# Kernel optimization log

Hardware: AMD Instinct MI355X
Metric: run time of the kernel (lower is better)

## Reference

```python
import jax, jax.numpy as jnp
import numpy as np

B, N, D, H, WIN = 8, 4096, 768, 8, 8
HD = D // H
FG = N // 2 + 1
FL = WIN // 2 + 1


def _gelu(x):
    return jax.nn.gelu(x, approximate=False)


def _cgelu(z):
    # magnitude-based complex GELU: z * gelu(|z|) / (|z| + 1e-6)
    mag = jnp.abs(z)
    return z * (_gelu(mag) / (mag + 1e-6))


def setup_inputs():
    key = jax.random.key(0)
    ks = jax.random.split(key, 8)

    def w(k, shape):
        return jax.random.normal(k, shape, dtype=jnp.float32) * 0.02

    return {
        "x": jax.random.normal(ks[0], (B, N, D), dtype=jnp.float32),
        "ln_w": jnp.ones((D,), jnp.float32),
        "ln_b": jnp.zeros((D,), jnp.float32),
        "bf_g": jnp.ones((H, FG, 1), jnp.float32),
        "bb_g": jnp.full((H, FG, 1), -0.1, jnp.float32),
        "bf_l": jnp.ones((H, FL, 1), jnp.float32),
        "bb_l": jnp.full((H, FL, 1), -0.1, jnp.float32),
        "w1g": w(ks[1], (D, D)),
        "b1g": jnp.zeros((D,), jnp.float32),
        "w2g": w(ks[2], (D, H * FG * 2)),
        "b2g": jnp.zeros((H * FG * 2,), jnp.float32),
        "w1l": w(ks[3], (D, D)),
        "b1l": jnp.zeros((D,), jnp.float32),
        "w2l": w(ks[4], (D, H * FL * 2)),
        "b2l": jnp.zeros((H * FL * 2,), jnp.float32),
        "wf1": w(ks[5], (D, D // 2)),
        "bf1": jnp.zeros((D // 2,), jnp.float32),
        "wf2": w(ks[6], (D // 2, H)),
        "bf2": jnp.zeros((H,), jnp.float32),
    }


def reference(x, ln_w, ln_b, bf_g, bb_g, bf_l, bb_l, w1g, b1g, w2g, b2g,
              w1l, b1l, w2l, b2l, wf1, bf1, wf2, bf2):
    # pre-norm (LayerNorm, eps=1e-5)
    mu = jnp.mean(x, axis=-1, keepdims=True)
    var = jnp.mean((x - mu) ** 2, axis=-1, keepdims=True)
    xn = (x - mu) / jnp.sqrt(var + 1e-5) * ln_w + ln_b
    xh = xn.reshape(B, N, H, HD).transpose(0, 2, 1, 3)  # (B,H,N,HD)
    ctx = xn.mean(axis=1)  # (B,D)

    # ---- global branch: Hann-windowed rFFT over full sequence ----
    ag = (_gelu(ctx @ w1g + b1g) @ w2g + b2g).reshape(B, H, FG, 2)
    hann_g = jnp.hanning(N).astype(x.dtype)[None, None, :, None]
    Ff = jnp.fft.rfft(xh * hann_g, axis=2, norm="ortho")  # (B,H,FG,HD) complex
    eff_f = bf_g[None] * (1.0 + ag[..., 0:1])
    eff_b = bb_g[None] + ag[..., 1:2]
    x_global = jnp.fft.irfft(_cgelu(Ff * eff_f + eff_b), n=N, axis=2, norm="ortho")

    al = (_gelu(ctx @ w1l + b1l) @ w2l + b2l).reshape(B, H, FL, 2)
    nw = N // WIN
    hann_l = jnp.hanning(WIN).astype(x.dtype)[None, None, None, :, None]
    xw = xh.reshape(B, H, nw, WIN, HD) * hann_l
    Fl_fft = jnp.fft.rfft(xw, axis=3, norm="ortho")  # (B,H,nw,FL,HD)
    eff_fl = bf_l[None, :, None] * (1.0 + al[:, :, None, :, 0:1])
    eff_bl = bb_l[None, :, None] + al[:, :, None, :, 1:2]
    x_local = jnp.fft.irfft(_cgelu(Fl_fft * eff_fl + eff_bl), n=WIN, axis=3,
                            norm="ortho").reshape(B, H, N, HD)

    # ---- fusion gate ----
    alpha = jax.nn.sigmoid(_gelu(ctx @ wf1 + bf1) @ wf2 + bf2).reshape(B, H, 1, 1)
    fused = alpha * x_global + (1.0 - alpha) * x_local
    return x + fused.transpose(0, 2, 1, 3).reshape(B, N, D)
```

## Files before the change

### kernel.cpp

```cpp
#include <hip/hip_runtime.h>
#include <math.h>

#define B_ 8
#define N_ 4096
#define D_ 768
#define H_ 8
#define HD_ 96
#define FG_ 2049
#define TWO_PI 6.283185307179586476925f
#define SWZ(i) ((i) ^ (((i) >> 4) & 15))

__device__ __forceinline__ float erf_fast(float x) {
    float ax = fabsf(x);
    float t = __builtin_amdgcn_rcpf(fmaf(0.3275911f, ax, 1.0f));
    float p = fmaf(fmaf(fmaf(fmaf(1.061405429f, t, -1.453152027f), t, 1.421413741f),
                        t, -0.284496736f), t, 0.254829592f) * t;
    float r = 1.0f - p * __expf(-ax * ax);
    return copysignf(r, x);
}

__device__ __forceinline__ float gelu_f(float x) {
    return 0.5f * x * (1.0f + erf_fast(x * 0.7071067811865475f));
}

__device__ __forceinline__ int rev4_12(int x) {
    int r = (int)(__brev((unsigned)x) >> 20);
    return ((r & 0x555) << 1) | ((r >> 1) & 0x555);
}

__global__ void k_init(const float* __restrict__ b2g, const float* __restrict__ b2l,
                       const float* __restrict__ b1g, const float* __restrict__ b1l,
                       float2* __restrict__ twg, float* __restrict__ hanng,
                       float* __restrict__ ctx, float* __restrict__ ag,
                       float* __restrict__ al, float* __restrict__ h1g,
                       float* __restrict__ h1l) {
    int i = blockIdx.x * 256 + threadIdx.x;
    if (i < 2048) {
        float s, c;
        sincosf(-TWO_PI * (float)i / 4096.0f, &s, &c);
        twg[i] = make_float2(c, s);
    }
    if (i < 4096) hanng[i] = 0.5f - 0.5f * cosf(TWO_PI * (float)i / 4095.0f);
    if (i < B_ * D_) ctx[i] = 0.f;
    if (i < 768) {
        float vg = b1g[i], vl = b1l[i];
        for (int b = 0; b < B_; ++b) {
            h1g[b * 768 + i] = vg;
            h1l[b * 768 + i] = vl;
        }
    }
    const int CG = H_ * FG_ * 2;
    if (i < CG) {
        float v = b2g[i];
        for (int b = 0; b < B_; ++b) ag[(size_t)b * CG + i] = v;
    } else if (i < CG + 80) {
        int cc = i - CG;
        float v = b2l[cc];
        for (int b = 0; b < B_; ++b) al[b * 80 + cc] = v;
    }
}

__global__ __launch_bounds__(256) void k_stats(const float* __restrict__ x,
                                               float* __restrict__ mu,
                                               float* __restrict__ rstd) {
    int row = blockIdx.x * 4 + (threadIdx.x >> 6);
    int lane = threadIdx.x & 63;
    const float4* xr = (const float4*)(x + (size_t)row * D_);
    float4 a = xr[lane], b = xr[lane + 64], c = xr[lane + 128];
    float s = a.x + a.y + a.z + a.w + b.x + b.y + b.z + b.w + c.x + c.y + c.z + c.w;
    #pragma unroll
    for (int o = 32; o > 0; o >>= 1) s += __shfl_xor(s, o);
    float m = s * (1.0f / 768.0f);
    float v = 0.f, d;
    d = a.x - m; v += d * d; d = a.y - m; v += d * d;
    d = a.z - m; v += d * d; d = a.w - m; v += d * d;
    d = b.x - m; v += d * d; d = b.y - m; v += d * d;
    d = b.z - m; v += d * d; d = b.w - m; v += d * d;
    d = c.x - m; v += d * d; d = c.y - m; v += d * d;
    d = c.z - m; v += d * d; d = c.w - m; v += d * d;
    #pragma unroll
    for (int o = 32; o > 0; o >>= 1) v += __shfl_xor(v, o);
    if (lane == 0) {
        mu[row] = m;
        rstd[row] = rsqrtf(v * (1.0f / 768.0f) + 1e-5f);
    }
}

__global__ __launch_bounds__(256) void k_lnT(const float* __restrict__ x,
                                             const float* __restrict__ mu,
                                             const float* __restrict__ rstd,
                                             const float* __restrict__ lw,
                                             const float* __restrict__ lb,
                                             float* __restrict__ xt,
                                             float* __restrict__ ctx) {
    __shared__ float tile[64][65];
    __shared__ float csum[4][64];
    int d0 = blockIdx.x * 64, n0 = blockIdx.y * 64, b = blockIdx.z;
    int c = threadIdx.x & 63, r4 = threadIdx.x >> 6;
    float w = lw[d0 + c], bias = lb[d0 + c];
    float partial = 0.f;
    #pragma unroll
    for (int q = 0; q < 16; ++q) {
        int r = r4 * 16 + q;
        int row = b * N_ + n0 + r;
        float v = (x[(size_t)row * D_ + d0 + c] - mu[row]) * rstd[row] * w + bias;
        tile[r][c] = v;
        partial += v;
    }
    csum[r4][c] = partial;
    __syncthreads();
    if (r4 == 0)
        atomicAdd(ctx + b * D_ + d0 + c,
                  (csum[0][c] + csum[1][c] + csum[2][c] + csum[3][c]) * (1.0f / 4096.0f));
    #pragma unroll
    for (int q = 0; q < 16; ++q) {
        int r = r4 * 16 + q;
        xt[((size_t)b * D_ + d0 + r) * N_ + n0 + c] = tile[c][r];
    }
}

__global__ void k_mlp1(const float* __restrict__ ctx,
                       const float* __restrict__ w1g, const float* __restrict__ w1l,
                       const float* __restrict__ wf1, const float* __restrict__ bf1,
                       float* __restrict__ h1g, float* __restrict__ h1l,
                       float* __restrict__ hf) {
    int t = threadIdx.x, xb = blockIdx.x, y = blockIdx.y;
    float acc[B_];
    #pragma unroll
    for (int b = 0; b < B_; ++b) acc[b] = 0.f;
    if (y < 8) {
        int c = xb * 256 + t;
        if (c >= 1536) return;
        const float* w = (c < 768) ? w1g : w1l;
        float* out = (c < 768) ? h1g : h1l;
        int cc = (c < 768) ? c : c - 768;
        int d0 = y * 96;
        for (int d = 0; d < 96; ++d) {
            float wv = w[(size_t)(d0 + d) * 768 + cc];
            #pragma unroll
            for (int b = 0; b < B_; ++b) acc[b] += ctx[b * 768 + d0 + d] * wv;
        }
        for (int b = 0; b < B_; ++b) atomicAdd(out + b * 768 + cc, acc[b]);
    } else {
        if (xb < 6) return;
        int cc = (xb - 6) * 256 + t;
        if (cc >= 384) return;
        for (int d = 0; d < 768; ++d) {
            float wv = wf1[(size_t)d * 384 + cc];
            #pragma unroll
            for (int b = 0; b < B_; ++b) acc[b] += ctx[b * 768 + d] * wv;
        }
        float bv = bf1[cc];
        for (int b = 0; b < B_; ++b) hf[b * 384 + cc] = gelu_f(acc[b] + bv);
    }
}

__global__ void k_mlp2(const float* __restrict__ h1g, const float* __restrict__ h1l,
                       const float* __restrict__ hf,
                       const float* __restrict__ w2g, const float* __restrict__ w2l,
                       const float* __restrict__ wf2, const float* __restrict__ bf2,
                       float* __restrict__ ag, float* __restrict__ al, float* __restrict__ gate) {
    int kc = blockIdx.y;
    int d0 = kc * 96;
    __shared__ float lg[B_ * 96];
    __shared__ float ll[B_ * 96];
    for (int i = threadIdx.x; i < B_ * 96; i += 256) {
        int bb = i / 96, dd = i % 96;
        lg[i] = gelu_f(h1g[bb * 768 + d0 + dd]);
        ll[i] = gelu_f(h1l[bb * 768 + d0 + dd]);
    }
    __syncthreads();
    int c = blockIdx.x * 256 + threadIdx.x;
    const int CG = H_ * FG_ * 2;
    float acc[B_];
    #pragma unroll
    for (int b = 0; b < B_; ++b) acc[b] = 0.f;
    if (c < CG) {
        for (int d = 0; d < 96; ++d) {
            float wv = w2g[(size_t)(d0 + d) * CG + c];
            #pragma unroll
            for (int b = 0; b < B_; ++b) acc[b] += lg[b * 96 + d] * wv;
        }
        for (int b = 0; b < B_; ++b) atomicAdd(ag + (size_t)b * CG + c, acc[b]);
    } else if (c < CG + 80) {
        int cc = c - CG;
        for (int d = 0; d < 96; ++d) {
            float wv = w2l[(d0 + d) * 80 + cc];
            #pragma unroll
            for (int b = 0; b < B_; ++b) acc[b] += ll[b * 96 + d] * wv;
        }
        for (int b = 0; b < B_; ++b) atomicAdd(al + b * 80 + cc, acc[b]);
    } else if (c < CG + 88 && kc == 0) {
        int cc = c - CG - 80;
        for (int d = 0; d < 384; ++d) {
            float wv = wf2[d * 8 + cc];
            #pragma unroll
            for (int b = 0; b < B_; ++b) acc[b] += hf[b * 384 + d] * wv;
        }
        for (int b = 0; b < B_; ++b)
            gate[b * 8 + cc] = 1.0f / (1.0f + expf(-(acc[b] + bf2[cc])));
    }
}

template<int LQ>
__device__ __forceinline__ void dit_stage_f(float2* z, const float2* __restrict__ twg, int t) {
    const int Q = 1 << LQ;
    #pragma unroll
    for (int u = 0; u < 4; ++u) {
        int j = t + (u << 8);
        int pos = j & (Q - 1);
        int i0 = ((j >> LQ) << (LQ + 2)) + pos;
        int p0 = SWZ(i0), p1 = SWZ(i0 + Q), p2 = SWZ(i0 + 2 * Q), p3 = SWZ(i0 + 3 * Q);
        float2 a = z[p0], b = z[p1], c = z[p2], d = z[p3];
        float2 w1 = twg[pos << (10 - LQ)];
        float2 w2 = make_float2(w1.x * w1.x - w1.y * w1.y, 2.f * w1.x * w1.y);
        float2 w3 = make_float2(w1.x * w2.x - w1.y * w2.y, w1.x * w2.y + w1.y * w2.x);
        float2 bh = make_float2(b.x * w1.x - b.y * w1.y, b.x * w1.y + b.y * w1.x);
        float2 ch = make_float2(c.x * w2.x - c.y * w2.y, c.x * w2.y + c.y * w2.x);
        float2 dh = make_float2(d.x * w3.x - d.y * w3.y, d.x * w3.y + d.y * w3.x);
        float t0x = a.x + ch.x,  t0y = a.y + ch.y;
        float t1x = a.x - ch.x,  t1y = a.y - ch.y;
        float t2x = bh.x + dh.x, t2y = bh.y + dh.y;
        float t3x = bh.x - dh.x, t3y = bh.y - dh.y;
        z[p0] = make_float2(t0x + t2x, t0y + t2y);
        z[p1] = make_float2(t1x + t3y, t1y - t3x);
        z[p2] = make_float2(t0x - t2x, t0y - t2y);
        z[p3] = make_float2(t1x - t3y, t1y + t3x);
    }
}

template<int LQ>
__device__ __forceinline__ void dif_stage_i(float2* z, const float2* __restrict__ twg, int t) {
    const int Q = 1 << LQ;
    #pragma unroll
    for (int u = 0; u < 4; ++u) {
        int j = t + (u << 8);
        int pos = j & (Q - 1);
        int i0 = ((j >> LQ) << (LQ + 2)) + pos;
        int p0 = SWZ(i0), p1 = SWZ(i0 + Q), p2 = SWZ(i0 + 2 * Q), p3 = SWZ(i0 + 3 * Q);
        float2 a = z[p0], b = z[p1], c = z[p2], d = z[p3];
        float t0x = a.x + c.x,  t0y = a.y + c.y;
        float t1x = a.x - c.x,  t1y = a.y - c.y;
        float t2x = b.x + d.x,  t2y = b.y + d.y;
        float t3x = b.x - d.x,  t3y = b.y - d.y;
        float2 w1 = twg[pos << (10 - LQ)];
        w1.y = -w1.y;
        float2 w2 = make_float2(w1.x * w1.x - w1.y * w1.y, 2.f * w1.x * w1.y);
        float2 w3 = make_float2(w1.x * w2.x - w1.y * w2.y, w1.x * w2.y + w1.y * w2.x);
        z[p0] = make_float2(t0x + t2x, t0y + t2y);
        float y1x = t1x - t3y, y1y = t1y + t3x;
        z[p1] = make_float2(y1x * w1.x - y1y * w1.y, y1x * w1.y + y1y * w1.x);
        float y2x = t0x - t2x, y2y = t0y - t2y;
        z[p2] = make_float2(y2x * w2.x - y2y * w2.y, y2x * w2.y + y2y * w2.x);
        float y3x = t1x + t3y, y3y = t1y - t3x;
        z[p3] = make_float2(y3x * w3.x - y3y * w3.y, y3x * w3.y + y3y * w3.x);
    }
}

#define W16C_INIT {1.f, 0.9238795325f, 0.7071067812f, 0.3826834324f, 0.f, \
                   -0.3826834324f, -0.7071067812f, -0.9238795325f, -1.f, -0.9238795325f}
#define W16S_INIT {0.f, -0.3826834324f, -0.7071067812f, -0.9238795325f, -1.f, \
                   -0.9238795325f, -0.7071067812f, -0.3826834324f, 0.f, 0.3826834324f}

__device__ __forceinline__ void fwd16_dit(float2* v) {
    #pragma unroll
    for (int g = 0; g < 4; ++g) {
        float2 a = v[4*g], b = v[4*g+1], c = v[4*g+2], d = v[4*g+3];
        float t0x = a.x + c.x, t0y = a.y + c.y, t1x = a.x - c.x, t1y = a.y - c.y;
        float t2x = b.x + d.x, t2y = b.y + d.y, t3x = b.x - d.x, t3y = b.y - d.y;
        v[4*g]   = make_float2(t0x + t2x, t0y + t2y);
        v[4*g+1] = make_float2(t1x + t3y, t1y - t3x);
        v[4*g+2] = make_float2(t0x - t2x, t0y - t2y);
        v[4*g+3] = make_float2(t1x - t3y, t1y + t3x);
    }
    const float WC[10] = W16C_INIT;
    const float WS[10] = W16S_INIT;
    #pragma unroll
    for (int m = 0; m < 4; ++m) {
        float2 a = v[m];
        float2 b0 = v[m+4], c0 = v[m+8], d0 = v[m+12];
        float2 b = make_float2(b0.x*WC[m]   - b0.y*WS[m],   b0.x*WS[m]   + b0.y*WC[m]);
        float2 c = make_float2(c0.x*WC[2*m] - c0.y*WS[2*m], c0.x*WS[2*m] + c0.y*WC[2*m]);
        float2 d = make_float2(d0.x*WC[3*m] - d0.y*WS[3*m], d0.x*WS[3*m] + d0.y*WC[3*m]);
        float t0x = a.x + c.x, t0y = a.y + c.y, t1x = a.x - c.x, t1y = a.y - c.y;
        float t2x = b.x + d.x, t2y = b.y + d.y, t3x = b.x - d.x, t3y = b.y - d.y;
        v[m]    = make_float2(t0x + t2x, t0y + t2y);
        v[m+4]  = make_float2(t1x + t3y, t1y - t3x);
        v[m+8]  = make_float2(t0x - t2x, t0y - t2y);
        v[m+12] = make_float2(t1x - t3y, t1y + t3x);
    }
}

__device__ __forceinline__ void inv16_dif(float2* v) {
    const float WC[10] = W16C_INIT;
    const float WS[10] = W16S_INIT;
    #pragma unroll
    for (int m = 0; m < 4; ++m) {
        float2 a = v[m], b = v[m+4], c = v[m+8], d = v[m+12];
        float t0x = a.x + c.x, t0y = a.y + c.y, t1x = a.x - c.x, t1y = a.y - c.y;
        float t2x = b.x + d.x, t2y = b.y + d.y, t3x = b.x - d.x, t3y = b.y - d.y;
        float y1x = t1x - t3y, y1y = t1y + t3x;
        float y2x = t0x - t2x, y2y = t0y - t2y;
        float y3x = t1x + t3y, y3y = t1y - t3x;
        v[m]    = make_float2(t0x + t2x, t0y + t2y);
        v[m+4]  = make_float2(y1x*WC[m]   + y1y*WS[m],   y1y*WC[m]   - y1x*WS[m]);
        v[m+8]  = make_float2(y2x*WC[2*m] + y2y*WS[2*m], y2y*WC[2*m] - y2x*WS[2*m]);
        v[m+12] = make_float2(y3x*WC[3*m] + y3y*WS[3*m], y3y*WC[3*m] - y3x*WS[3*m]);
    }
    #pragma unroll
    for (int g = 0; g < 4; ++g) {
        float2 a = v[4*g], b = v[4*g+1], c = v[4*g+2], d = v[4*g+3];
        float t0x = a.x + c.x, t0y = a.y + c.y, t1x = a.x - c.x, t1y = a.y - c.y;
        float t2x = b.x + d.x, t2y = b.y + d.y, t3x = b.x - d.x, t3y = b.y - d.y;
        v[4*g]   = make_float2(t0x + t2x, t0y + t2y);
        v[4*g+1] = make_float2(t1x - t3y, t1y + t3x);
        v[4*g+2] = make_float2(t0x - t2x, t0y - t2y);
        v[4*g+3] = make_float2(t1x + t3y, t1y - t3x);
    }
}

__global__ __launch_bounds__(256) void k_spectral(
        const float* __restrict__ xt,
        const float* __restrict__ ag,
        const float* __restrict__ al,
        const float* __restrict__ gate,
        const float* __restrict__ bf_g, const float* __restrict__ bb_g,
        const float* __restrict__ bf_l, const float* __restrict__ bb_l,
        const float2* __restrict__ twg, const float* __restrict__ hanng,
        float* __restrict__ fused)
{
    __shared__ float2 z[4096];
    int line0 = blockIdx.x * 2;
    int d0 = line0 % 768, b = line0 / 768;
    int h = d0 / HD_;
    int t = threadIdx.x;

    const float* src0 = xt + (size_t)line0 * N_;
    const float* src1 = src0 + N_;
    float raw0[16], raw1[16];
    #pragma unroll
    for (int q = 0; q < 4; ++q) {
        float4 v0 = ((const float4*)src0)[t * 4 + q];
        float4 v1 = ((const float4*)src1)[t * 4 + q];
        raw0[q * 4 + 0] = v0.x; raw0[q * 4 + 1] = v0.y;
        raw0[q * 4 + 2] = v0.z; raw0[q * 4 + 3] = v0.w;
        raw1[q * 4 + 0] = v1.x; raw1[q * 4 + 1] = v1.y;
        raw1[q * 4 + 2] = v1.z; raw1[q * 4 + 3] = v1.w;
    }
    #pragma unroll
    for (int q = 0; q < 4; ++q) {
        float4 hw = ((const float4*)hanng)[t * 4 + q];
        int nb = t * 16 + q * 4;
        z[SWZ(rev4_12(nb + 0))] = make_float2(raw0[q*4+0] * hw.x, raw1[q*4+0] * hw.x);
        z[SWZ(rev4_12(nb + 1))] = make_float2(raw0[q*4+1] * hw.y, raw1[q*4+1] * hw.y);
        z[SWZ(rev4_12(nb + 2))] = make_float2(raw0[q*4+2] * hw.z, raw1[q*4+2] * hw.z);
        z[SWZ(rev4_12(nb + 3))] = make_float2(raw0[q*4+3] * hw.w, raw1[q*4+3] * hw.w);
    }

    float alc = gate[b * 8 + h];
    const float* alb = al + b * 80;
    float effl_f[5], effl_b[5];
    #pragma unroll
    for (int f = 0; f < 5; ++f) {
        int idx = h * 5 + f;
        effl_f[f] = bf_l[idx] * (1.0f + alb[idx * 2]);
        effl_b[f] = bb_l[idx] + alb[idx * 2 + 1];
    }
    const float s8 = 0.3535533905932738f;
    const float c7 = 0.7071067811865476f;
    const float cosT[8] = {1.f, c7, 0.f, -c7, -1.f, -c7, 0.f, c7};
    const float sinT[8] = {0.f, c7, 1.f, c7, 0.f, -c7, -1.f, -c7};
    const float hl[8] = {0.f, 0.18825510f, 0.61126047f, 0.95048444f,
                         0.95048444f, 0.61126047f, 0.18825510f, 0.f};
    float xl0[16], xl1[16];
    #pragma unroll
    for (int ln = 0; ln < 2; ++ln) {
        float* rawp = ln ? raw1 : raw0;
        float* xlp  = ln ? xl1 : xl0;
        #pragma unroll
        for (int w2 = 0; w2 < 2; ++w2) {
            float xw[8];
            #pragma unroll
            for (int j = 0; j < 8; ++j) xw[j] = rawp[w2 * 8 + j] * hl[j];
            float Yr[5], Yi[5];
            #pragma unroll
            for (int f = 0; f < 5; ++f) {
                float fr = 0.f, fi = 0.f;
                #pragma unroll
                for (int j = 0; j < 8; ++j) {
                    int k8 = (f * j) & 7;
                    fr += xw[j] * cosT[k8];
                    fi -= xw[j] * sinT[k8];
                }
                fr *= s8; fi *= s8;
                float zr = fr * effl_f[f] + effl_b[f];
                float zi = fi * effl_f[f];
                float mag = sqrtf(zr * zr + zi * zi);
                float g = gelu_f(mag) * __builtin_amdgcn_rcpf(mag + 1e-6f);
                Yr[f] = zr * g; Yi[f] = zi * g;
            }
            #pragma unroll
            for (int j = 0; j < 8; ++j) {
                float acc = Yr[0] + Yr[4] * ((j & 1) ? -1.f : 1.f);
                #pragma unroll
                for (int f = 1; f < 4; ++f) {
                    int k8 = (f * j) & 7;
                    acc += 2.f * (Yr[f] * cosT[k8] - Yi[f] * sinT[k8]);
                }
                xlp[w2 * 8 + j] = acc * s8;
            }
        }
    }

    __syncthreads();
    {
        float2 v[16];
        #pragma unroll
        for (int i = 0; i < 16; ++i) v[i] = z[SWZ(t * 16 + i)];
        fwd16_dit(v);
        #pragma unroll
        for (int i = 0; i < 16; ++i) z[SWZ(t * 16 + i)] = v[i];
    }
    __syncthreads();
    dit_stage_f<4>(z, twg, t);  __syncthreads();
    dit_stage_f<6>(z, twg, t);  __syncthreads();
    dit_stage_f<8>(z, twg, t);  __syncthreads();
    dit_stage_f<10>(z, twg, t); __syncthreads();

    const float inv64 = 1.0f / 64.0f;
    const float* agb = ag + (size_t)b * 32784;
    for (int k = t; k < 2048; k += 256) {
        int km = (4096 - k) & 4095;
        int pk = SWZ(k), pm = SWZ(km);
        float2 Z = z[pk], Z2 = z[pm];
        float X0r = 0.5f * (Z.x + Z2.x), X0i = 0.5f * (Z.y - Z2.y);
        float X1r = 0.5f * (Z.y + Z2.y), X1i = -0.5f * (Z.x - Z2.x);
        int idx = h * FG_ + k;
        float efff = bf_g[idx] * (1.0f + agb[idx * 2]);
        float effb = bb_g[idx] + agb[idx * 2 + 1];
        float z0r = X0r * inv64 * efff + effb, z0i = X0i * inv64 * efff;
        float m0 = sqrtf(z0r * z0r + z0i * z0i);
        float g0 = gelu_f(m0) * __builtin_amdgcn_rcpf(m0 + 1e-6f);
        float Y0r = z0r * g0, Y0i = z0i * g0;
        float z1r = X1r * inv64 * efff + effb, z1i = X1i * inv64 * efff;
        float m1 = sqrtf(z1r * z1r + z1i * z1i);
        float g1 = gelu_f(m1) * __builtin_amdgcn_rcpf(m1 + 1e-6f);
        float Y1r = z1r * g1, Y1i = z1i * g1;
        z[pk] = make_float2(Y0r - Y1i, Y0i + Y1r);
        if (k) z[pm] = make_float2(Y0r + Y1i, Y1r - Y0i);
    }
    if (t == 0) {
        int pk = SWZ(2048);
        float2 Z = z[pk];
        int idx = h * FG_ + 2048;
        float efff = bf_g[idx] * (1.0f + agb[idx * 2]);
        float effb = bb_g[idx] + agb[idx * 2 + 1];
        float z0r = Z.x * inv64 * efff + effb;
        float m0 = fabsf(z0r);
        float Y0r = z0r * (gelu_f(m0) * __builtin_amdgcn_rcpf(m0 + 1e-6f));
        float z1r = Z.y * inv64 * efff + effb;
        float m1 = fabsf(z1r);
        float Y1r = z1r * (gelu_f(m1) * __builtin_amdgcn_rcpf(m1 + 1e-6f));
        z[pk] = make_float2(Y0r, Y1r);
    }
    __syncthreads();

    dif_stage_i<10>(z, twg, t); __syncthreads();
    dif_stage_i<8>(z, twg, t);  __syncthreads();
    dif_stage_i<6>(z, twg, t);  __syncthreads();
    dif_stage_i<4>(z, twg, t);  __syncthreads();
    {
        float2 v[16];
        #pragma unroll
        for (int i = 0; i < 16; ++i) v[i] = z[SWZ(t * 16 + i)];
        inv16_dif(v);
        #pragma unroll
        for (int i = 0; i < 16; ++i) z[SWZ(t * 16 + i)] = v[i];
    }
    __syncthreads();

    float* dst0 = fused + (size_t)line0 * N_;
    float* dst1 = dst0 + N_;
    float one_m = 1.0f - alc;
    #pragma unroll
    for (int q = 0; q < 4; ++q) {
        int base = t * 16 + q * 4;
        float2 za = z[SWZ(rev4_12(base + 0))], zb = z[SWZ(rev4_12(base + 1))];
        float2 zc = z[SWZ(rev4_12(base + 2))], zd = z[SWZ(rev4_12(base + 3))];
        float4 v0 = make_float4(alc * za.x * inv64 + one_m * xl0[q * 4 + 0],
                                alc * zb.x * inv64 + one_m * xl0[q * 4 + 1],
                                alc * zc.x * inv64 + one_m * xl0[q * 4 + 2],
                                alc * zd.x * inv64 + one_m * xl0[q * 4 + 3]);
        float4 v1 = make_float4(alc * za.y * inv64 + one_m * xl1[q * 4 + 0],
                                alc * zb.y * inv64 + one_m * xl1[q * 4 + 1],
                                alc * zc.y * inv64 + one_m * xl1[q * 4 + 2],
                                alc * zd.y * inv64 + one_m * xl1[q * 4 + 3]);
        ((float4*)dst0)[t * 4 + q] = v0;
        ((float4*)dst1)[t * 4 + q] = v1;
    }
}

__global__ void k_addout(const float* __restrict__ fused, const float* __restrict__ x,
                         float* __restrict__ out) {
    __shared__ float tile[64][65];
    int d0 = blockIdx.x * 64, n0 = blockIdx.y * 64, b = blockIdx.z;
    int c = threadIdx.x & 63, r4 = threadIdx.x >> 6;
    for (int q = 0; q < 16; ++q) {
        int r = r4 * 16 + q;
        tile[r][c] = fused[((size_t)b * D_ + d0 + r) * N_ + n0 + c];
    }
    __syncthreads();
    for (int q = 0; q < 16; ++q) {
        int r = r4 * 16 + q;
        size_t o = ((size_t)b * N_ + n0 + r) * D_ + d0 + c;
        out[o] = x[o] + tile[c][r];
    }
}

extern "C" void kernel_launch(void* const* d_in, const int* in_sizes, int n_in,
                              void* d_out, int out_size, void* d_ws, size_t ws_size,
                              hipStream_t stream) {
    const float* x    = (const float*)d_in[0];
    const float* ln_w = (const float*)d_in[1];
    const float* ln_b = (const float*)d_in[2];
    const float* bf_g = (const float*)d_in[3];
    const float* bb_g = (const float*)d_in[4];
    const float* bf_l = (const float*)d_in[5];
    const float* bb_l = (const float*)d_in[6];
    const float* w1g  = (const float*)d_in[7];
    const float* b1g  = (const float*)d_in[8];
    const float* w2g  = (const float*)d_in[9];
    const float* b2g  = (const float*)d_in[10];
    const float* w1l  = (const float*)d_in[11];
    const float* b1l  = (const float*)d_in[12];
    const float* w2l  = (const float*)d_in[13];
    const float* b2l  = (const float*)d_in[14];
    const float* wf1  = (const float*)d_in[15];
    const float* bf1  = (const float*)d_in[16];
    const float* wf2  = (const float*)d_in[17];
    const float* bf2  = (const float*)d_in[18];
    float* out = (float*)d_out;

    char* ws = (char*)d_ws;
    const size_t big = (size_t)B_ * D_ * N_ * sizeof(float);
    float* XT  = (float*)ws; ws += big;
    float* FU  = (float*)ws; ws += big;
    float* ctx = (float*)ws; ws += (size_t)B_ * D_ * 4;
    float* h1g = (float*)ws; ws += (size_t)B_ * 768 * 4;
    float* h1l = (float*)ws; ws += (size_t)B_ * 768 * 4;
    float* hf  = (float*)ws; ws += (size_t)B_ * 384 * 4;
    float* ag  = (float*)ws; ws += (size_t)B_ * 32784 * 4;
    float* alb = (float*)ws; ws += (size_t)B_ * 80 * 4;
    float* gat = (float*)ws; ws += (size_t)B_ * 8 * 4;
    float2* twg = (float2*)ws; ws += 2048 * sizeof(float2);
    float* hanng = (float*)ws; ws += 4096 * sizeof(float);
    float* mu   = FU;
    float* rstd = FU + 32768;

    k_init<<<129, 256, 0, stream>>>(b2g, b2l, b1g, b1l, twg, hanng, ctx, ag, alb,
                                    h1g, h1l);
    k_stats<<<8192, 256, 0, stream>>>(x, mu, rstd);
    k_lnT<<<dim3(12, 64, 8), 256, 0, stream>>>(x, mu, rstd, ln_w, ln_b, XT, ctx);
    k_mlp1<<<dim3(8, 9), 256, 0, stream>>>(ctx, w1g, w1l, wf1, bf1, h1g, h1l, hf);
    k_mlp2<<<dim3(129, 8), 256, 0, stream>>>(h1g, h1l, hf, w2g, w2l, wf2, bf2, ag, alb, gat);
    k_spectral<<<B_ * D_ / 2, 256, 0, stream>>>(XT, ag, alb, gat, bf_g, bb_g, bf_l, bb_l,
                                                twg, hanng, FU);
    k_addout<<<dim3(12, 64, 8), 256, 0, stream>>>(FU, x, out);
}
```

Measured before the change: 625.0 us.

## Fuse LayerNorm stats into transpose, pair radix-4 FFT stages, closed-form 8-point DFT

Removes the separate statistics kernel by computing row mean and variance inside the transpose kernel. Each block now handles one 64-row slab across all 12 column tiles, using a one-pass sum/sum-of-squares variance. The radix-4 FFT stages are merged in pairs, so each thread does a 16-point radix-16 pass in registers, halving the shared-memory passes and barriers. The local 8-point windowed DFT and its inverse become explicit butterfly formulas instead of table-driven loops. In exchange, the transpose kernel launches far fewer blocks, the FFT uses more registers, and the one-pass variance can lose precision.

```diff
diff --git a/kernel.cpp b/kernel.cpp
--- a/kernel.cpp
+++ b/kernel.cpp
@@ -9,6 +9,10 @@
 #define FG_ 2049
 #define TWO_PI 6.283185307179586476925f
 #define SWZ(i) ((i) ^ (((i) >> 4) & 15))
+
+__device__ __forceinline__ float2 cmul(float2 a, float2 b) {
+    return make_float2(a.x * b.x - a.y * b.y, a.x * b.y + a.y * b.x);
+}
 
 __device__ __forceinline__ float erf_fast(float x) {
     float ax = fabsf(x);
@@ -60,62 +64,58 @@
     }
 }
 
-__global__ __launch_bounds__(256) void k_stats(const float* __restrict__ x,
-                                               float* __restrict__ mu,
-                                               float* __restrict__ rstd) {
-    int row = blockIdx.x * 4 + (threadIdx.x >> 6);
-    int lane = threadIdx.x & 63;
-    const float4* xr = (const float4*)(x + (size_t)row * D_);
-    float4 a = xr[lane], b = xr[lane + 64], c = xr[lane + 128];
-    float s = a.x + a.y + a.z + a.w + b.x + b.y + b.z + b.w + c.x + c.y + c.z + c.w;
-    #pragma unroll
-    for (int o = 32; o > 0; o >>= 1) s += __shfl_xor(s, o);
-    float m = s * (1.0f / 768.0f);
-    float v = 0.f, d;
-    d = a.x - m; v += d * d; d = a.y - m; v += d * d;
-    d = a.z - m; v += d * d; d = a.w - m; v += d * d;
-    d = b.x - m; v += d * d; d = b.y - m; v += d * d;
-    d = b.z - m; v += d * d; d = b.w - m; v += d * d;
-    d = c.x - m; v += d * d; d = c.y - m; v += d * d;
-    d = c.z - m; v += d * d; d = c.w - m; v += d * d;
-    #pragma unroll
-    for (int o = 32; o > 0; o >>= 1) v += __shfl_xor(v, o);
-    if (lane == 0) {
-        mu[row] = m;
-        rstd[row] = rsqrtf(v * (1.0f / 768.0f) + 1e-5f);
-    }
-}
-
 __global__ __launch_bounds__(256) void k_lnT(const float* __restrict__ x,
-                                             const float* __restrict__ mu,
-                                             const float* __restrict__ rstd,
                                              const float* __restrict__ lw,
                                              const float* __restrict__ lb,
                                              float* __restrict__ xt,
                                              float* __restrict__ ctx) {
     __shared__ float tile[64][65];
     __shared__ float csum[4][64];
-    int d0 = blockIdx.x * 64, n0 = blockIdx.y * 64, b = blockIdx.z;
-    int c = threadIdx.x & 63, r4 = threadIdx.x >> 6;
-    float w = lw[d0 + c], bias = lb[d0 + c];
-    float partial = 0.f;
-    #pragma unroll
-    for (int q = 0; q < 16; ++q) {
-        int r = r4 * 16 + q;
-        int row = b * N_ + n0 + r;
-        float v = (x[(size_t)row * D_ + d0 + c] - mu[row]) * rstd[row] * w + bias;
-        tile[r][c] = v;
-        partial += v;
-    }
-    csum[r4][c] = partial;
+    __shared__ float mus[64], rstds[64];
+    int n0 = blockIdx.x * 64, b = blockIdx.y;
+    int t = threadIdx.x;
+    {
+        int r = t >> 2, sub = t & 3;
+        const float4* rowp = (const float4*)(x + ((size_t)(b * N_ + n0 + r)) * D_) + sub * 48;
+        float s = 0.f, s2 = 0.f;
+        #pragma unroll 4
+        for (int i = 0; i < 48; ++i) {
+            float4 v = rowp[i];
+            s += v.x + v.y + v.z + v.w;
+            s2 += v.x * v.x + v.y * v.y + v.z * v.z + v.w * v.w;
+        }
+        s += __shfl_xor(s, 1);  s += __shfl_xor(s, 2);
+        s2 += __shfl_xor(s2, 1); s2 += __shfl_xor(s2, 2);
+        if (sub == 0) {
+            float m = s * (1.0f / 768.0f);
+            mus[r] = m;
+            rstds[r] = rsqrtf(s2 * (1.0f / 768.0f) - m * m + 1e-5f);
+        }
+    }
     __syncthreads();
-    if (r4 == 0)
-        atomicAdd(ctx + b * D_ + d0 + c,
-                  (csum[0][c] + csum[1][c] + csum[2][c] + csum[3][c]) * (1.0f / 4096.0f));
-    #pragma unroll
-    for (int q = 0; q < 16; ++q) {
-        int r = r4 * 16 + q;
-        xt[((size_t)b * D_ + d0 + r) * N_ + n0 + c] = tile[c][r];
+    int c = t & 63, r4 = t >> 6;
+    for (int dt = 0; dt < 12; ++dt) {
+        int d0 = dt * 64;
+        float wv = lw[d0 + c], bv = lb[d0 + c];
+        float partial = 0.f;
+        #pragma unroll
+        for (int q = 0; q < 16; ++q) {
+            int r = r4 * 16 + q;
+            float v = (x[((size_t)(b * N_ + n0 + r)) * D_ + d0 + c] - mus[r]) * rstds[r] * wv + bv;
+            tile[r][c] = v;
+            partial += v;
+        }
+        csum[r4][c] = partial;
+        __syncthreads();
+        if (r4 == 0)
+            atomicAdd(ctx + b * D_ + d0 + c,
+                      (csum[0][c] + csum[1][c] + csum[2][c] + csum[3][c]) * (1.0f / 4096.0f));
+        #pragma unroll
+        for (int q = 0; q < 16; ++q) {
+            int r = r4 * 16 + q;
+            xt[((size_t)b * D_ + d0 + r) * N_ + n0 + c] = tile[c][r];
+        }
+        __syncthreads();
     }
 }
 
@@ -203,58 +203,103 @@
 }
 
 template<int LQ>
-__device__ __forceinline__ void dit_stage_f(float2* z, const float2* __restrict__ twg, int t) {
+__device__ __forceinline__ void dit_pair_f(float2* z, const float2* __restrict__ twg, int t) {
     const int Q = 1 << LQ;
-    #pragma unroll
-    for (int u = 0; u < 4; ++u) {
-        int j = t + (u << 8);
-        int pos = j & (Q - 1);
-        int i0 = ((j >> LQ) << (LQ + 2)) + pos;
-        int p0 = SWZ(i0), p1 = SWZ(i0 + Q), p2 = SWZ(i0 + 2 * Q), p3 = SWZ(i0 + 3 * Q);
-        float2 a = z[p0], b = z[p1], c = z[p2], d = z[p3];
-        float2 w1 = twg[pos << (10 - LQ)];
-        float2 w2 = make_float2(w1.x * w1.x - w1.y * w1.y, 2.f * w1.x * w1.y);
-        float2 w3 = make_float2(w1.x * w2.x - w1.y * w2.y, w1.x * w2.y + w1.y * w2.x);
-        float2 bh = make_float2(b.x * w1.x - b.y * w1.y, b.x * w1.y + b.y * w1.x);
-        float2 ch = make_float2(c.x * w2.x - c.y * w2.y, c.x * w2.y + c.y * w2.x);
-        float2 dh = make_float2(d.x * w3.x - d.y * w3.y, d.x * w3.y + d.y * w3.x);
-        float t0x = a.x + ch.x,  t0y = a.y + ch.y;
-        float t1x = a.x - ch.x,  t1y = a.y - ch.y;
-        float t2x = bh.x + dh.x, t2y = bh.y + dh.y;
-        float t3x = bh.x - dh.x, t3y = bh.y - dh.y;
-        z[p0] = make_float2(t0x + t2x, t0y + t2y);
-        z[p1] = make_float2(t1x + t3y, t1y - t3x);
-        z[p2] = make_float2(t0x - t2x, t0y - t2y);
-        z[p3] = make_float2(t1x - t3y, t1y + t3x);
-    }
+    int lo = t & (Q - 1);
+    int base = ((t >> LQ) << (LQ + 4)) + lo;
+    float2 v[16];
+    #pragma unroll
+    for (int b = 0; b < 4; ++b)
+        #pragma unroll
+        for (int a = 0; a < 4; ++a)
+            v[b * 4 + a] = z[SWZ(base + (b << (LQ + 2)) + (a << LQ))];
+    {
+        float2 w1 = twg[lo << (10 - LQ)];
+        float2 w2 = cmul(w1, w1), w3 = cmul(w1, w2);
+        #pragma unroll
+        for (int b = 0; b < 4; ++b) {
+            float2 A = v[b*4+0], Bv = cmul(v[b*4+1], w1);
+            float2 C = cmul(v[b*4+2], w2), Dv = cmul(v[b*4+3], w3);
+            float t0x = A.x + C.x,  t0y = A.y + C.y;
+            float t1x = A.x - C.x,  t1y = A.y - C.y;
+            float t2x = Bv.x + Dv.x, t2y = Bv.y + Dv.y;
+            float t3x = Bv.x - Dv.x, t3y = Bv.y - Dv.y;
+            v[b*4+0] = make_float2(t0x + t2x, t0y + t2y);
+            v[b*4+1] = make_float2(t1x + t3y, t1y - t3x);
+            v[b*4+2] = make_float2(t0x - t2x, t0y - t2y);
+            v[b*4+3] = make_float2(t1x - t3y, t1y + t3x);
+        }
+    }
+    #pragma unroll
+    for (int a = 0; a < 4; ++a) {
+        float2 u1 = twg[(a * Q + lo) << (8 - LQ)];
+        float2 u2 = cmul(u1, u1), u3 = cmul(u1, u2);
+        float2 A = v[0*4+a], Bv = cmul(v[1*4+a], u1);
+        float2 C = cmul(v[2*4+a], u2), Dv = cmul(v[3*4+a], u3);
+        float t0x = A.x + C.x,  t0y = A.y + C.y;
+        float t1x = A.x - C.x,  t1y = A.y - C.y;
+        float t2x = Bv.x + Dv.x, t2y = Bv.y + Dv.y;
+        float t3x = Bv.x - Dv.x, t3y = Bv.y - Dv.y;
+        v[0*4+a] = make_float2(t0x + t2x, t0y + t2y);
+        v[1*4+a] = make_float2(t1x + t3y, t1y - t3x);
+        v[2*4+a] = make_float2(t0x - t2x, t0y - t2y);
+        v[3*4+a] = make_float2(t1x - t3y, t1y + t3x);
+    }
+    #pragma unroll
+    for (int b = 0; b < 4; ++b)
+        #pragma unroll
+        for (int a = 0; a < 4; ++a)
+            z[SWZ(base + (b << (LQ + 2)) + (a << LQ))] = v[b * 4 + a];
 }
 
 template<int LQ>
-__device__ __forceinline__ void dif_stage_i(float2* z, const float2* __restrict__ twg, int t) {
+__device__ __forceinline__ void dif_pair_i(float2* z, const float2* __restrict__ twg, int t) {
     const int Q = 1 << LQ;
-    #pragma unroll
-    for (int u = 0; u < 4; ++u) {
-        int j = t + (u << 8);
-        int pos = j & (Q - 1);
-        int i0 = ((j >> LQ) << (LQ + 2)) + pos;
-        int p0 = SWZ(i0), p1 = SWZ(i0 + Q), p2 = SWZ(i0 + 2 * Q), p3 = SWZ(i0 + 3 * Q);
-        float2 a = z[p0], b = z[p1], c = z[p2], d = z[p3];
-        float t0x = a.x + c.x,  t0y = a.y + c.y;
-        float t1x = a.x - c.x,  t1y = a.y - c.y;
-        float t2x = b.x + d.x,  t2y = b.y + d.y;
-        float t3x = b.x - d.x,  t3y = b.y - d.y;
-        float2 w1 = twg[pos << (10 - LQ)];
+    int lo = t & (Q - 1);
+    int base = ((t >> LQ) << (LQ + 4)) + lo;
+    float2 v[16];
+    #pragma unroll
+    for (int b = 0; b < 4; ++b)
+        #pragma unroll
+        for (int a = 0; a < 4; ++a)
+            v[b * 4 + a] = z[SWZ(base + (b << (LQ + 2)) + (a << LQ))];
+    #pragma unroll
+    for (int a = 0; a < 4; ++a) {
+        float2 A = v[0*4+a], Bv = v[1*4+a], C = v[2*4+a], Dv = v[3*4+a];
+        float t0x = A.x + C.x,  t0y = A.y + C.y;
+        float t1x = A.x - C.x,  t1y = A.y - C.y;
+        float t2x = Bv.x + Dv.x, t2y = Bv.y + Dv.y;
+        float t3x = Bv.x - Dv.x, t3y = Bv.y - Dv.y;
+        float2 u1 = twg[(a * Q + lo) << (8 - LQ)];
+        u1.y = -u1.y;
+        float2 u2 = cmul(u1, u1), u3 = cmul(u1, u2);
+        v[0*4+a] = make_float2(t0x + t2x, t0y + t2y);
+        v[1*4+a] = cmul(make_float2(t1x - t3y, t1y + t3x), u1);
+        v[2*4+a] = cmul(make_float2(t0x - t2x, t0y - t2y), u2);
+        v[3*4+a] = cmul(make_float2(t1x + t3y, t1y - t3x), u3);
+    }
+    {
+        float2 w1 = twg[lo << (10 - LQ)];
         w1.y = -w1.y;
-        float2 w2 = make_float2(w1.x * w1.x - w1.y * w1.y, 2.f * w1.x * w1.y);
-        float2 w3 = make_float2(w1.x * w2.x - w1.y * w2.y, w1.x * w2.y + w1.y * w2.x);
-        z[p0] = make_float2(t0x + t2x, t0y + t2y);
-        float y1x = t1x - t3y, y1y = t1y + t3x;
-        z[p1] = make_float2(y1x * w1.x - y1y * w1.y, y1x * w1.y + y1y * w1.x);
-        float y2x = t0x - t2x, y2y = t0y - t2y;
-        z[p2] = make_float2(y2x * w2.x - y2y * w2.y, y2x * w2.y + y2y * w2.x);
-        float y3x = t1x + t3y, y3y = t1y - t3x;
-        z[p3] = make_float2(y3x * w3.x - y3y * w3.y, y3x * w3.y + y3y * w3.x);
-    }
+        float2 w2 = cmul(w1, w1), w3 = cmul(w1, w2);
+        #pragma unroll
+        for (int b = 0; b < 4; ++b) {
+            float2 A = v[b*4+0], Bv = v[b*4+1], C = v[b*4+2], Dv = v[b*4+3];
+            float t0x = A.x + C.x,  t0y = A.y + C.y;
+            float t1x = A.x - C.x,  t1y = A.y - C.y;
+            float t2x = Bv.x + Dv.x, t2y = Bv.y + Dv.y;
+            float t3x = Bv.x - Dv.x, t3y = Bv.y - Dv.y;
+            v[b*4+0] = make_float2(t0x + t2x, t0y + t2y);
+            v[b*4+1] = cmul(make_float2(t1x - t3y, t1y + t3x), w1);
+            v[b*4+2] = cmul(make_float2(t0x - t2x, t0y - t2y), w2);
+            v[b*4+3] = cmul(make_float2(t1x + t3y, t1y - t3x), w3);
+        }
+    }
+    #pragma unroll
+    for (int b = 0; b < 4; ++b)
+        #pragma unroll
+        for (int a = 0; a < 4; ++a)
+            z[SWZ(base + (b << (LQ + 2)) + (a << LQ))] = v[b * 4 + a];
 }
 
 #define W16C_INIT {1.f, 0.9238795325f, 0.7071067812f, 0.3826834324f, 0.f, \
@@ -359,19 +404,16 @@
 
     float alc = gate[b * 8 + h];
     const float* alb = al + b * 80;
-    float effl_f[5], effl_b[5];
+    const float s8 = 0.3535533905932738f;
+    const float c7 = 0.7071067811865476f;
+    float sfl[5], effl_b[5];
     #pragma unroll
     for (int f = 0; f < 5; ++f) {
         int idx = h * 5 + f;
-        effl_f[f] = bf_l[idx] * (1.0f + alb[idx * 2]);
+        sfl[f] = bf_l[idx] * (1.0f + alb[idx * 2]) * s8;
         effl_b[f] = bb_l[idx] + alb[idx * 2 + 1];
     }
-    const float s8 = 0.3535533905932738f;
-    const float c7 = 0.7071067811865476f;
-    const float cosT[8] = {1.f, c7, 0.f, -c7, -1.f, -c7, 0.f, c7};
-    const float sinT[8] = {0.f, c7, 1.f, c7, 0.f, -c7, -1.f, -c7};
-    const float hl[8] = {0.f, 0.18825510f, 0.61126047f, 0.95048444f,
-                         0.95048444f, 0.61126047f, 0.18825510f, 0.f};
+    const float H1 = 0.18825510f, H2 = 0.61126047f, H3 = 0.95048444f;
     float xl0[16], xl1[16];
     #pragma unroll
     for (int ln = 0; ln < 2; ++ln) {
@@ -379,36 +421,65 @@
         float* xlp  = ln ? xl1 : xl0;
         #pragma unroll
         for (int w2 = 0; w2 < 2; ++w2) {
-            float xw[8];
-            #pragma unroll
-            for (int j = 0; j < 8; ++j) xw[j] = rawp[w2 * 8 + j] * hl[j];
-            float Yr[5], Yi[5];
-            #pragma unroll
-            for (int f = 0; f < 5; ++f) {
-                float fr = 0.f, fi = 0.f;
-                #pragma unroll
-                for (int j = 0; j < 8; ++j) {
-                    int k8 = (f * j) & 7;
-                    fr += xw[j] * cosT[k8];
-                    fi -= xw[j] * sinT[k8];
-                }
-                fr *= s8; fi *= s8;
-                float zr = fr * effl_f[f] + effl_b[f];
-                float zi = fi * effl_f[f];
-                float mag = sqrtf(zr * zr + zi * zi);
-                float g = gelu_f(mag) * __builtin_amdgcn_rcpf(mag + 1e-6f);
-                Yr[f] = zr * g; Yi[f] = zi * g;
+            const float* r = rawp + w2 * 8;
+            float x1 = r[1] * H1, x2 = r[2] * H2, x3 = r[3] * H3;
+            float x4 = r[4] * H3, x5 = r[5] * H2, x6 = r[6] * H1;
+            float s26 = x2 + x6, d26 = x2 - x6;
+            float s15 = x1 + x5, d15 = x1 - x5;
+            float E0 = x4 + s26, E2 = x4 - s26;
+            float E1r = -x4, E1i = -d26;
+            float O0 = s15 + x3, O2 = s15 - x3;
+            float O1r = d15, O1i = -x3;
+            float X0 = E0 + O0;
+            float X4 = E0 - O0;
+            float X2r = E2, X2i = -O2;
+            float pp = c7 * (O1r + O1i), qq = c7 * (O1i - O1r);
+            float X1r = E1r + pp, X1i = E1i + qq;
+            float X3r = E1r - pp, X3i = qq - E1i;
+            float Y0r, Y1r, Y1i, Y2r, Y2i, Y3r, Y3i, Y4r;
+            {
+                float zr = X0 * sfl[0] + effl_b[0];
+                float m = fabsf(zr);
+                Y0r = zr * (gelu_f(m) * __builtin_amdgcn_rcpf(m + 1e-6f));
             }
-            #pragma unroll
-            for (int j = 0; j < 8; ++j) {
-                float acc = Yr[0] + Yr[4] * ((j & 1) ? -1.f : 1.f);
-                #pragma unroll
-                for (int f = 1; f < 4; ++f) {
-                    int k8 = (f * j) & 7;
-                    acc += 2.f * (Yr[f] * cosT[k8] - Yi[f] * sinT[k8]);
-                }
-                xlp[w2 * 8 + j] = acc * s8;
+            {
+                float zr = X1r * sfl[1] + effl_b[1], zi = X1i * sfl[1];
+                float m = sqrtf(zr * zr + zi * zi);
+                float g = gelu_f(m) * __builtin_amdgcn_rcpf(m + 1e-6f);
+                Y1r = zr * g; Y1i = zi * g;
             }
+            {
+                float zr = X2r * sfl[2] + effl_b[2], zi = X2i * sfl[2];
+                float m = sqrtf(zr * zr + zi * zi);
+                float g = gelu_f(m) * __builtin_amdgcn_rcpf(m + 1e-6f);
+                Y2r = zr * g; Y2i = zi * g;
+            }
+            {
+                float zr = X3r * sfl[3] + effl_b[3], zi = X3i * sfl[3];
+                float m = sqrtf(zr * zr + zi * zi);
+                float g = gelu_f(m) * __builtin_amdgcn_rcpf(m + 1e-6f);
+                Y3r = zr * g; Y3i = zi * g;
+            }
+            {
+                float zr = X4 * sfl[4] + effl_b[4];
+                float m = fabsf(zr);
+                Y4r = zr * (gelu_f(m) * __builtin_amdgcn_rcpf(m + 1e-6f));
+            }
+            float iE0 = 0.5f * (Y0r + Y4r), iO0 = 0.5f * (Y0r - Y4r);
+            float iE2 = Y2r, iO2 = -Y2i;
+            float iE1r = 0.5f * (Y1r + Y3r), iE1i = 0.5f * (Y1i - Y3i);
+            float Pr = 0.5f * (Y1r - Y3r), Pi = 0.5f * (Y1i + Y3i);
+            float iO1r = c7 * (Pr - Pi), iO1i = c7 * (Pr + Pi);
+            float ae = iE0 + iE2, be = iE0 - iE2;
+            float ao = iO0 + iO2, bo = iO0 - iO2;
+            xlp[w2*8 + 0] = c7 * (ae + 2.f * iE1r);
+            xlp[w2*8 + 2] = c7 * (be - 2.f * iE1i);
+            xlp[w2*8 + 4] = c7 * (ae - 2.f * iE1r);
+            xlp[w2*8 + 6] = c7 * (be + 2.f * iE1i);
+            xlp[w2*8 + 1] = c7 * (ao + 2.f * iO1r);
+            xlp[w2*8 + 3] = c7 * (bo - 2.f * iO1i);
+            xlp[w2*8 + 5] = c7 * (ao - 2.f * iO1r);
+            xlp[w2*8 + 7] = c7 * (bo + 2.f * iO1i);
         }
     }
 
@@ -422,10 +493,8 @@
         for (int i = 0; i < 16; ++i) z[SWZ(t * 16 + i)] = v[i];
     }
     __syncthreads();
-    dit_stage_f<4>(z, twg, t);  __syncthreads();
-    dit_stage_f<6>(z, twg, t);  __syncthreads();
-    dit_stage_f<8>(z, twg, t);  __syncthreads();
-    dit_stage_f<10>(z, twg, t); __syncthreads();
+    dit_pair_f<4>(z, twg, t);  __syncthreads();
+    dit_pair_f<8>(z, twg, t);  __syncthreads();
 
     const float inv64 = 1.0f / 64.0f;
     const float* agb = ag + (size_t)b * 32784;
@@ -465,10 +534,8 @@
     }
     __syncthreads();
 
-    dif_stage_i<10>(z, twg, t); __syncthreads();
-    dif_stage_i<8>(z, twg, t);  __syncthreads();
-    dif_stage_i<6>(z, twg, t);  __syncthreads();
-    dif_stage_i<4>(z, twg, t);  __syncthreads();
+    dif_pair_i<8>(z, twg, t);  __syncthreads();
+    dif_pair_i<4>(z, twg, t);  __syncthreads();
     {
         float2 v[16];
         #pragma unroll
@@ -554,13 +621,10 @@
     float* gat = (float*)ws; ws += (size_t)B_ * 8 * 4;
     float2* twg = (float2*)ws; ws += 2048 * sizeof(float2);
     float* hanng = (float*)ws; ws += 4096 * sizeof(float);
-    float* mu   = FU;
-    float* rstd = FU + 32768;
 
     k_init<<<129, 256, 0, stream>>>(b2g, b2l, b1g, b1l, twg, hanng, ctx, ag, alb,
                                     h1g, h1l);
-    k_stats<<<8192, 256, 0, stream>>>(x, mu, rstd);
-    k_lnT<<<dim3(12, 64, 8), 256, 0, stream>>>(x, mu, rstd, ln_w, ln_b, XT, ctx);
+    k_lnT<<<dim3(64, 8), 256, 0, stream>>>(x, ln_w, ln_b, XT, ctx);
     k_mlp1<<<dim3(8, 9), 256, 0, stream>>>(ctx, w1g, w1l, wf1, bf1, h1g, h1l, hf);
     k_mlp2<<<dim3(129, 8), 256, 0, stream>>>(h1g, h1l, hf, w2g, w2l, wf2, bf2, ag, alb, gat);
     k_spectral<<<B_ * D_ / 2, 256, 0, stream>>>(XT, ag, alb, gat, bf_g, bb_g, bf_l, bb_l,
```

New measurement: 615.2 us. No clear change (-1.6%).
